# Performance work log

Measured on AMD Instinct MI355X. Metric: run time of the kernel, lower is better.

## Reference

```python
import jax, jax.numpy as jnp
import numpy as np

NBIN = 25
DELTA = 2.0 / (NBIN - 1)
EPS_COS = 1e-8   # torch CosineSimilarity eps
EPS_P = 1e-16    # pNumerator init in original


def setup_inputs() -> dict:
    key = jax.random.key(0)
    k1, k2, k3 = jax.random.split(key, 3)
    B, N, M = 16, 50000, 128
    qX = jax.random.normal(k1, (B, M), dtype=jnp.float32)
    dXs = jax.random.normal(k2, (B, N, M), dtype=jnp.float32)
    labels = jax.random.randint(k3, (B, N), 0, 2, dtype=jnp.int32)
    return {"qX": qX, "dXs": dXs, "labels": labels}


def _qap(qX, dXs, labels_f):
    # cosine similarity, matching torch.nn.CosineSimilarity (norms clamped at eps)
    num = jnp.einsum("bm,bnm->bn", qX, dXs)                      # (B, N)
    qn = jnp.maximum(jnp.linalg.norm(qX, axis=-1), EPS_COS)      # (B,)
    dn = jnp.maximum(jnp.linalg.norm(dXs, axis=-1), EPS_COS)     # (B, N)
    sim = num / (qn[:, None] * dn)                               # (B, N)

    # soft assignment to NBIN triangular bins centered at 1 - m*DELTA
    centers = 1.0 - jnp.arange(NBIN, dtype=sim.dtype) * DELTA    # (NBIN,)
    sa = jnp.clip(1.0 - jnp.abs(sim[..., None] - centers) / DELTA, 0.0)  # (B, N, NBIN)

    # per-bin reductions (computed once), then cumulative sums replace the O(nBin^2) loop
    num_per_bin = jnp.einsum("bnk,bn->bk", sa, labels_f)         # dot(sa[:,n], labels)
    den_per_bin = jnp.sum(sa, axis=1)                            # dot(sa[:,n], ones)

    pDen = jnp.cumsum(num_per_bin, axis=1)                       # (B, NBIN)
    pNum = EPS_P + jnp.cumsum(den_per_bin, axis=1)
    precision = pDen / pNum
    recall = num_per_bin / jnp.sum(labels_f, axis=1, keepdims=True)

    ap = jnp.sum(precision * recall, axis=1)                     # (B,)
    return jnp.mean(ap)


def reference(qX, dXs, labels):
    labels_f = labels.astype(qX.dtype)
    return _qap(qX, dXs, labels_f)
```

## Files before the change

### kernel.cpp

```cpp
#include <hip/hip_runtime.h>
#include <math.h>

#define NBIN 25
#define T 256
#define PAD 27
#define ROWS_PER_CHUNK 384
#define ACC_ROWS 64


__global__ __launch_bounds__(256, 8)
void qap_accum(const float* __restrict__ qX, const float* __restrict__ dXs,
               const int* __restrict__ labels, float* __restrict__ ws,
               int N, int nChunks) {
    __shared__ float accN[ACC_ROWS * PAD];
    __shared__ float accD[ACC_ROWS * PAD];
    __shared__ float labLds[ROWS_PER_CHUNK];
    __shared__ float part[4 * 64];

    const int tid  = threadIdx.x;
    const int b    = blockIdx.x / nChunks;
    const int chunk= blockIdx.x % nChunks;
    const int wave = tid >> 6;
    const int lane = tid & 63;
    const int half = lane >> 5;
    const int sub  = lane & 31;

    const int n0   = chunk * ROWS_PER_CHUNK;
    const int n1   = min(n0 + ROWS_PER_CHUNK, N);
    const int rows = n1 - n0;

    for (int i = tid; i < ACC_ROWS * PAD; i += T) { accN[i] = 0.f; accD[i] = 0.f; }
    for (int i = tid; i < rows; i += T)
        labLds[i] = (float)labels[(size_t)b * N + n0 + i];

    const float4 qv = reinterpret_cast<const float4*>(qX + b * 128)[sub];
    float qs = qv.x*qv.x + qv.y*qv.y + qv.z*qv.z + qv.w*qv.w;
    #pragma unroll
    for (int mk = 1; mk <= 16; mk <<= 1) qs += __shfl_xor(qs, mk);
    const float qn = fmaxf(sqrtf(qs), 1e-8f);
    __syncthreads();

    float labCnt = 0.f;
    const int accRowBase = (wave << 4) + (half << 3);
    const float* dbase = dXs + (size_t)b * N * 128;

    int r = n0 + (wave << 1) + half;
    bool act = r < n1;
    float4 x = make_float4(0.f, 0.f, 0.f, 0.f);
    if (act) x = reinterpret_cast<const float4*>(dbase + (size_t)r * 128)[sub];

    int it = 0;
    while (act) {
        const int rn = r + 8;
        const bool actn = rn < n1;
        float4 xn = make_float4(0.f, 0.f, 0.f, 0.f);
        if (actn) xn = reinterpret_cast<const float4*>(dbase + (size_t)rn * 128)[sub];

        float dot = x.x*qv.x + x.y*qv.y + x.z*qv.z + x.w*qv.w;
        float nr  = x.x*x.x  + x.y*x.y  + x.z*x.z  + x.w*x.w;
        #pragma unroll
        for (int mk = 1; mk <= 16; mk <<= 1) {
            dot += __shfl_xor(dot, mk);
            nr  += __shfl_xor(nr,  mk);
        }
        if (sub == (it & 7)) {
            const float dn  = fmaxf(sqrtf(nr), 1e-8f);
            const float sim = dot / (qn * dn);
            float p = fminf(fmaxf((1.f - sim) * 12.f, 0.f), 24.f);
            int m = (int)p; if (m > 24) m = 24;
            const float frac = p - (float)m;
            const float lab  = labLds[r - n0];
            labCnt += lab;
            const float w0 = 1.f - frac;
            const int ba = (accRowBase + sub) * PAD;
            accD[ba + m] += w0;
            accN[ba + m] += lab * w0;
            if (m + 1 < NBIN) {
                accD[ba + m + 1] += frac;
                accN[ba + m + 1] += lab * frac;
            }
        }
        r = rn; act = actn; x = xn; ++it;
    }
    if (sub < 8) accD[(accRowBase + sub) * PAD + 25] = labCnt;
    __syncthreads();

    const int c = tid & 63, g = tid >> 6;
    if (c < 51) {
        const int idx = (c < 25) ? c : ((c < 50) ? (c - 25) : 25);
        const float* arr = (c < 25) ? accN : accD;
        float s = 0.f;
        #pragma unroll
        for (int t = g * 16; t < g * 16 + 16; ++t) s += arr[t * PAD + idx];
        part[g * 64 + c] = s;
    }
    __syncthreads();
    if (tid < 51)
        atomicAdd(&ws[b * 64 + tid],
                  part[tid] + part[64 + tid] + part[128 + tid] + part[192 + tid]);
}

__global__ void qap_final(const float* __restrict__ ws, float* __restrict__ out, int B) {
    const int lane = threadIdx.x;
    float ap = 0.f;
    if (lane < B) {
        const float* w = ws + lane * 64;
        const float labSum = w[50];
        float cn = 0.f, cd = 0.f;
        for (int k = 0; k < NBIN; ++k) {
            const float nk = w[k];
            const float dk = w[25 + k];
            cn += nk;
            cd += dk;
            const float prec = cn / (1e-16f + cd);
            const float rec  = nk / labSum;
            ap = fmaf(prec, rec, ap);
        }
    }
    for (int off = 32; off > 0; off >>= 1) ap += __shfl_down(ap, off);
    if (lane == 0) out[0] = ap / (float)B;
}

extern "C" void kernel_launch(void* const* d_in, const int* in_sizes, int n_in,
                              void* d_out, int out_size, void* d_ws, size_t ws_size,
                              hipStream_t stream) {
    const float* qX     = (const float*)d_in[0];
    const float* dXs    = (const float*)d_in[1];
    const int*   labels = (const int*)d_in[2];
    float* out = (float*)d_out;
    float* ws  = (float*)d_ws;

    const int M = in_sizes[1] / in_sizes[2];
    const int B = in_sizes[0] / M;
    const int N = in_sizes[2] / B;
    (void)M;

    const int nChunks = (N + ROWS_PER_CHUNK - 1) / ROWS_PER_CHUNK;

    hipMemsetAsync(ws, 0, (size_t)B * 64 * sizeof(float), stream);
    qap_accum<<<B * nChunks, T, 0, stream>>>(qX, dXs, labels, ws, N, nChunks);
    qap_final<<<1, 64, 0, stream>>>(ws, out, B);
}
```

Baseline: 579.9 us.

## Unroll row processing by four with batched prefetch and shared shuffle reductions

Each half-wave now works on four rows per iteration. The four float4 loads for the next group are prefetched ahead of time, and the dot-product and norm shuffle reductions for all four rows are interleaved, so latency is hidden and the binning step uses four lanes instead of one. Chunk size grows from 384 to 512 rows, the per-lane accumulator rows shrink to 32, and the occupancy hint drops from 8 to 4 blocks. The cost is more registers per thread and fewer blocks in flight, which could reduce latency hiding on what is a memory-bound stream.

Result: faster. 556.4 us (-4.0%).

```diff
diff --git a/kernel.cpp b/kernel.cpp
--- a/kernel.cpp
+++ b/kernel.cpp
@@ -4,32 +4,31 @@
 #define NBIN 25
 #define T 256
 #define PAD 27
-#define ROWS_PER_CHUNK 384
-#define ACC_ROWS 64
+#define RPC 512
+#define UNROLL 4
+#define GROUPS (RPC / (8 * UNROLL))
 
 
-__global__ __launch_bounds__(256, 8)
+__global__ __launch_bounds__(256, 4)
 void qap_accum(const float* __restrict__ qX, const float* __restrict__ dXs,
                const int* __restrict__ labels, float* __restrict__ ws,
                int N, int nChunks) {
-    __shared__ float accN[ACC_ROWS * PAD];
-    __shared__ float accD[ACC_ROWS * PAD];
-    __shared__ float labLds[ROWS_PER_CHUNK];
+    __shared__ float accN[32 * PAD];
+    __shared__ float accD[32 * PAD];
+    __shared__ float labLds[RPC];
     __shared__ float part[4 * 64];
 
-    const int tid  = threadIdx.x;
-    const int b    = blockIdx.x / nChunks;
-    const int chunk= blockIdx.x % nChunks;
-    const int wave = tid >> 6;
-    const int lane = tid & 63;
-    const int half = lane >> 5;
-    const int sub  = lane & 31;
+    const int tid     = threadIdx.x;
+    const int b       = blockIdx.x / nChunks;
+    const int chunk   = blockIdx.x % nChunks;
+    const int sub     = tid & 31;
+    const int halfIdx = tid >> 5;
 
-    const int n0   = chunk * ROWS_PER_CHUNK;
-    const int n1   = min(n0 + ROWS_PER_CHUNK, N);
+    const int n0   = chunk * RPC;
+    const int n1   = min(n0 + RPC, N);
     const int rows = n1 - n0;
 
-    for (int i = tid; i < ACC_ROWS * PAD; i += T) { accN[i] = 0.f; accD[i] = 0.f; }
+    for (int i = tid; i < 32 * PAD; i += T) { accN[i] = 0.f; accD[i] = 0.f; }
     for (int i = tid; i < rows; i += T)
         labLds[i] = (float)labels[(size_t)b * N + n0 + i];
 
@@ -40,59 +39,89 @@
     const float qn = fmaxf(sqrtf(qs), 1e-8f);
     __syncthreads();
 
+    const float* dbase = dXs + (size_t)b * N * 128;
     float labCnt = 0.f;
-    const int accRowBase = (wave << 4) + (half << 3);
-    const float* dbase = dXs + (size_t)b * N * 128;
 
-    int r = n0 + (wave << 1) + half;
-    bool act = r < n1;
-    float4 x = make_float4(0.f, 0.f, 0.f, 0.f);
-    if (act) x = reinterpret_cast<const float4*>(dbase + (size_t)r * 128)[sub];
+    float4 xc[UNROLL], xn[UNROLL];
 
-    int it = 0;
-    while (act) {
-        const int rn = r + 8;
-        const bool actn = rn < n1;
-        float4 xn = make_float4(0.f, 0.f, 0.f, 0.f);
-        if (actn) xn = reinterpret_cast<const float4*>(dbase + (size_t)rn * 128)[sub];
+    #pragma unroll
+    for (int j = 0; j < UNROLL; ++j) {
+        const int r = n0 + halfIdx + 8 * j;
+        xc[j] = make_float4(0.f, 0.f, 0.f, 0.f);
+        if (r < n1)
+            xc[j] = reinterpret_cast<const float4*>(dbase + (size_t)r * 128)[sub];
+    }
 
-        float dot = x.x*qv.x + x.y*qv.y + x.z*qv.z + x.w*qv.w;
-        float nr  = x.x*x.x  + x.y*x.y  + x.z*x.z  + x.w*x.w;
+    #pragma unroll 1
+    for (int g = 0; g < GROUPS; ++g) {
+        if (g + 1 < GROUPS) {
+            #pragma unroll
+            for (int j = 0; j < UNROLL; ++j) {
+                const int r = n0 + halfIdx + 8 * (UNROLL * (g + 1) + j);
+                xn[j] = make_float4(0.f, 0.f, 0.f, 0.f);
+                if (r < n1)
+                    xn[j] = reinterpret_cast<const float4*>(dbase + (size_t)r * 128)[sub];
+            }
+        }
+
+        float dt[UNROLL], nr[UNROLL];
+        #pragma unroll
+        for (int j = 0; j < UNROLL; ++j) {
+            dt[j] = xc[j].x*qv.x + xc[j].y*qv.y + xc[j].z*qv.z + xc[j].w*qv.w;
+            nr[j] = xc[j].x*xc[j].x + xc[j].y*xc[j].y + xc[j].z*xc[j].z + xc[j].w*xc[j].w;
+        }
         #pragma unroll
         for (int mk = 1; mk <= 16; mk <<= 1) {
-            dot += __shfl_xor(dot, mk);
-            nr  += __shfl_xor(nr,  mk);
-        }
-        if (sub == (it & 7)) {
-            const float dn  = fmaxf(sqrtf(nr), 1e-8f);
-            const float sim = dot / (qn * dn);
-            float p = fminf(fmaxf((1.f - sim) * 12.f, 0.f), 24.f);
-            int m = (int)p; if (m > 24) m = 24;
-            const float frac = p - (float)m;
-            const float lab  = labLds[r - n0];
-            labCnt += lab;
-            const float w0 = 1.f - frac;
-            const int ba = (accRowBase + sub) * PAD;
-            accD[ba + m] += w0;
-            accN[ba + m] += lab * w0;
-            if (m + 1 < NBIN) {
-                accD[ba + m + 1] += frac;
-                accN[ba + m + 1] += lab * frac;
+            #pragma unroll
+            for (int j = 0; j < UNROLL; ++j) {
+                dt[j] += __shfl_xor(dt[j], mk);
+                nr[j] += __shfl_xor(nr[j], mk);
             }
         }
-        r = rn; act = actn; x = xn; ++it;
+
+        const float d01 = (sub & 1) ? dt[1] : dt[0];
+        const float d23 = (sub & 1) ? dt[3] : dt[2];
+        const float dsel = (sub & 2) ? d23 : d01;
+        const float n01 = (sub & 1) ? nr[1] : nr[0];
+        const float n23 = (sub & 1) ? nr[3] : nr[2];
+        const float nsel = (sub & 2) ? n23 : n01;
+
+        if (sub < UNROLL) {
+            const int r = n0 + halfIdx + 8 * (UNROLL * g + sub);
+            if (r < n1) {
+                const float dn  = fmaxf(sqrtf(nsel), 1e-8f);
+                const float sim = dsel / (qn * dn);
+                float p = fminf(fmaxf((1.f - sim) * 12.f, 0.f), 24.f);
+                int m = (int)p; if (m > 24) m = 24;
+                const float frac = p - (float)m;
+                const float lab  = labLds[r - n0];
+                labCnt += lab;
+                const float w0 = 1.f - frac;
+                const int ba = (halfIdx * 4 + sub) * PAD;
+                accD[ba + m] += w0;
+                accN[ba + m] += lab * w0;
+                if (m + 1 < NBIN) {
+                    accD[ba + m + 1] += frac;
+                    accN[ba + m + 1] += lab * frac;
+                }
+            }
+        }
+
+        #pragma unroll
+        for (int j = 0; j < UNROLL; ++j) xc[j] = xn[j];
     }
-    if (sub < 8) accD[(accRowBase + sub) * PAD + 25] = labCnt;
+
+    if (sub < UNROLL) accD[(halfIdx * 4 + sub) * PAD + 25] = labCnt;
     __syncthreads();
 
-    const int c = tid & 63, g = tid >> 6;
+    const int c = tid & 63, g4 = tid >> 6;
     if (c < 51) {
         const int idx = (c < 25) ? c : ((c < 50) ? (c - 25) : 25);
         const float* arr = (c < 25) ? accN : accD;
         float s = 0.f;
         #pragma unroll
-        for (int t = g * 16; t < g * 16 + 16; ++t) s += arr[t * PAD + idx];
-        part[g * 64 + c] = s;
+        for (int t = g4 * 8; t < g4 * 8 + 8; ++t) s += arr[t * PAD + idx];
+        part[g4 * 64 + c] = s;
     }
     __syncthreads();
     if (tid < 51)
@@ -135,7 +164,7 @@
     const int N = in_sizes[2] / B;
     (void)M;
 
-    const int nChunks = (N + ROWS_PER_CHUNK - 1) / ROWS_PER_CHUNK;
+    const int nChunks = (N + RPC - 1) / RPC;
 
     hipMemsetAsync(ws, 0, (size_t)B * 64 * sizeof(float), stream);
     qap_accum<<<B * nChunks, T, 0, stream>>>(qX, dXs, labels, ws, N, nChunks);
```
